# Performance work log

Measured on AMD Instinct MI355X. Metric: run time of the kernel, lower is better.

Reference implementation:

```python
import jax, jax.numpy as jnp
import numpy as np

H = 16   # n_heads == n_I
D = 64   # d_q = d_k = d_v = d_r
DX = H * D
B, S = 4, 2048

def setup_inputs() -> dict:
    key = jax.random.key(0)
    ks = jax.random.split(key, 9)
    sc = 0.02
    return {
        "value": jax.random.normal(ks[0], (B, S, DX), jnp.float32),
        "key":   jax.random.normal(ks[1], (B, S, DX), jnp.float32),
        "query": jax.random.normal(ks[2], (B, S, DX), jnp.float32),
        "Wq_w": jax.random.normal(ks[3], (DX, DX), jnp.float32) * sc,
        "Wq_b": jnp.zeros((DX,), jnp.float32),
        "Wk_w": jax.random.normal(ks[4], (DX, DX), jnp.float32) * sc,
        "Wk_b": jnp.zeros((DX,), jnp.float32),
        "Wv_w": jax.random.normal(ks[5], (DX, DX), jnp.float32) * sc,
        "Wv_b": jnp.zeros((DX,), jnp.float32),
        "Wr_w": jax.random.normal(ks[6], (DX, DX), jnp.float32) * sc,
        "Wr_b": jnp.zeros((DX,), jnp.float32),
        "Wout_w": jax.random.normal(ks[7], (DX, DX), jnp.float32) * sc,
        "Wout_b": jnp.zeros((DX,), jnp.float32),
    }

def _heads(x, b, s):
    # [b, s, H*D] -> [b, H, s, D]
    return x.reshape(b, s, H, D).transpose(0, 2, 1, 3)

def reference(value, key, query, Wq_w, Wq_b, Wk_w, Wk_b, Wv_w, Wv_b,
              Wr_w, Wr_b, Wout_w, Wout_b):
    b, s, _ = query.shape
    # torch nn.Linear: y = x @ W.T + b
    Q = _heads(query @ Wq_w.T + Wq_b, b, s)   # [b,H,s,D]
    K = _heads(key   @ Wk_w.T + Wk_b, b, s)
    V = _heads(value @ Wv_w.T + Wv_b, b, s)
    R = _heads(query @ Wr_w.T + Wr_b, b, s)
    dot_scale = jnp.sqrt(jnp.float32(D))
    scores = jnp.einsum("bhid,bhjd->bhij", Q, K) / dot_scale  # [b,H,s,s]
    attn = jax.nn.softmax(scores, axis=-1)                    # dropout p=0
    out = jnp.einsum("bhij,bhjd->bhid", attn, V)              # [b,H,s,D]
    out = out * R                                             # R-gating
    out = out.transpose(0, 2, 1, 3).reshape(b, s, H * D)
    return out @ Wout_w.T + Wout_b
```

## Files before the change

kernel.cpp:

```cpp
#include <hip/hip_runtime.h>
#include <hip/hip_bf16.h>

typedef __bf16 bf16;
typedef __bf16 bf16x4 __attribute__((ext_vector_type(4)));
typedef __bf16 bf16x8 __attribute__((ext_vector_type(8)));
typedef float  f32x4  __attribute__((ext_vector_type(4)));

#define MFMA_16x16x32(a, b, c) __builtin_amdgcn_mfma_f32_16x16x32_bf16((a), (b), (c), 0, 0, 0)

typedef const void __attribute__((address_space(1))) gvoid;
typedef void __attribute__((address_space(3))) svoid;

__device__ __forceinline__ void async_copy16(const void* gptr, void* ldsptr) {
    __builtin_amdgcn_global_load_lds((gvoid*)gptr, (svoid*)ldsptr, 16, 0, 0);
}

__device__ __forceinline__ int swz8(int row, int quad) {
    return (quad ^ ((row >> 1) & 3)) * 8;
}

__global__ void cvt3_acts(const float* __restrict__ s0, const float* __restrict__ s1,
                          const float* __restrict__ s2,
                          bf16* __restrict__ d0, bf16* __restrict__ d1, bf16* __restrict__ d2)
{
    constexpr int N4SEG = 8192 * 1024 / 4;
    int i = blockIdx.x * blockDim.x + threadIdx.x;
    const int stride = gridDim.x * blockDim.x;
    for (; i < 3 * N4SEG; i += stride) {
        const int seg = i / N4SEG;
        const int j = i - seg * N4SEG;
        const float* s = seg == 0 ? s0 : (seg == 1 ? s1 : s2);
        bf16* d = seg == 0 ? d0 : (seg == 1 ? d1 : d2);
        float4 v = ((const float4*)s)[j];
        bf16x4 o = { (bf16)v.x, (bf16)v.y, (bf16)v.z, (bf16)v.w };
        ((bf16x4*)d)[j] = o;
    }
}

__global__ void cvt5_wts(const float* __restrict__ s0, const float* __restrict__ s1,
                         const float* __restrict__ s2, const float* __restrict__ s3,
                         const float* __restrict__ s4,
                         bf16* __restrict__ d0, bf16* __restrict__ d1, bf16* __restrict__ d2,
                         bf16* __restrict__ d3, bf16* __restrict__ d4)
{
    constexpr int N4SEG = 1024 * 1024 / 4;
    int i = blockIdx.x * blockDim.x + threadIdx.x;
    const int stride = gridDim.x * blockDim.x;
    for (; i < 5 * N4SEG; i += stride) {
        const int seg = i / N4SEG;
        const int j = i - seg * N4SEG;
        const float* s = seg == 0 ? s0 : seg == 1 ? s1 : seg == 2 ? s2 : seg == 3 ? s3 : s4;
        bf16* d = seg == 0 ? d0 : seg == 1 ? d1 : seg == 2 ? d2 : seg == 3 ? d3 : d4;
        float4 v = ((const float4*)s)[j];
        bf16x4 o = { (bf16)v.x, (bf16)v.y, (bf16)v.z, (bf16)v.w };
        ((bf16x4*)d)[j] = o;
    }
}

__global__ void proj_fused(const bf16* __restrict__ xq, const bf16* __restrict__ xk,
                           const bf16* __restrict__ xv, const bf16* __restrict__ wall,
                           const float* __restrict__ ball,
                           bf16* __restrict__ qr, bf16* __restrict__ kws,
                           bf16* __restrict__ vtws)
{
    constexpr int K = 1024, SDIM = 2048;
    __shared__ alignas(16) bf16 As[2][128 * 32];
    __shared__ alignas(16) bf16 Bs[2][128 * 32];

    const int tid  = threadIdx.x;
    const int lane = tid & 63;
    const int wave = tid >> 6;
    const int wm   = wave >> 1;
    const int wn   = wave & 1;
    const int bm   = blockIdx.x * 128;
    const int by   = blockIdx.y;
    const int bn   = by * 128;
    const int l15  = lane & 15;
    const int quad = lane >> 4;

    const bf16* X = (by < 16) ? xq : (by < 24 ? xk : xv);

    const int srow = lane >> 2;
    const int scol = (lane & 3) * 8;

    const bf16* aseg0 = X + (size_t)(bm + wave * 32 + srow) * K + scol;
    const bf16* aseg1 = X + (size_t)(bm + wave * 32 + 16 + srow) * K + scol;
    const bf16* bseg0 = wall + (size_t)(bn + wave * 32 + srow) * K + scol;
    const bf16* bseg1 = wall + (size_t)(bn + wave * 32 + 16 + srow) * K + scol;

    f32x4 acc[4][4] = {};

    async_copy16(aseg0, As[0] + (wave * 2 + 0) * 512);
    async_copy16(aseg1, As[0] + (wave * 2 + 1) * 512);
    async_copy16(bseg0, Bs[0] + (wave * 2 + 0) * 512);
    async_copy16(bseg1, Bs[0] + (wave * 2 + 1) * 512);

    for (int k0 = 0; k0 < K; k0 += 32) {
        const int cur = (k0 >> 5) & 1;
        __syncthreads();
        if (k0 + 32 < K) {
            const int nxt = cur ^ 1;
            async_copy16(aseg0 + k0 + 32, As[nxt] + (wave * 2 + 0) * 512);
            async_copy16(aseg1 + k0 + 32, As[nxt] + (wave * 2 + 1) * 512);
            async_copy16(bseg0 + k0 + 32, Bs[nxt] + (wave * 2 + 0) * 512);
            async_copy16(bseg1 + k0 + 32, Bs[nxt] + (wave * 2 + 1) * 512);
        }

        bf16x8 af[4], bfr[4];
        #pragma unroll
        for (int i = 0; i < 4; ++i)
            af[i] = *(const bf16x8*)(As[cur] + (wm * 64 + i * 16 + l15) * 32 + quad * 8);
        #pragma unroll
        for (int j = 0; j < 4; ++j)
            bfr[j] = *(const bf16x8*)(Bs[cur] + (wn * 64 + j * 16 + l15) * 32 + quad * 8);
        #pragma unroll
        for (int i = 0; i < 4; ++i)
            #pragma unroll
            for (int j = 0; j < 4; ++j)
                acc[i][j] = MFMA_16x16x32(af[i], bfr[j], acc[i][j]);
    }

    #pragma unroll
    for (int i = 0; i < 4; ++i) {
        const int rowg = bm + wm * 64 + i * 16 + quad * 4;
        #pragma unroll
        for (int j = 0; j < 4; ++j) {
            const int colg = bn + wn * 64 + j * 16 + l15;
            const float bv = ball[colg];
            if (by < 16) {
                #pragma unroll
                for (int r = 0; r < 4; ++r)
                    qr[(size_t)(rowg + r) * 2048 + colg] = (bf16)(acc[i][j][r] + bv);
            } else if (by < 24) {
                const int cl = colg - 2048;
                #pragma unroll
                for (int r = 0; r < 4; ++r)
                    kws[(size_t)(rowg + r) * 1024 + cl] = (bf16)(acc[i][j][r] + bv);
            } else {
                const int d = colg - 3072;
                bf16x4 o;
                #pragma unroll
                for (int r = 0; r < 4; ++r) o[r] = (bf16)(acc[i][j][r] + bv);
                *(bf16x4*)(vtws + (size_t)(rowg >> 11) * 1024 * SDIM
                                + (size_t)d * SDIM + (rowg & (SDIM - 1))) = o;
            }
        }
    }
}

__global__ void gemm_out(const bf16* __restrict__ X, const bf16* __restrict__ W,
                         const float* __restrict__ bias, float* __restrict__ Y)
{
    constexpr int K = 1024, N = 1024;
    __shared__ alignas(16) bf16 As[2][128 * 32];
    __shared__ alignas(16) bf16 Bs[2][128 * 32];

    const int tid  = threadIdx.x;
    const int lane = tid & 63;
    const int wave = tid >> 6;
    const int wm   = wave >> 1;
    const int wn   = wave & 1;
    const int bm   = blockIdx.x * 128;
    const int bn   = blockIdx.y * 128;
    const int l15  = lane & 15;
    const int quad = lane >> 4;

    const int srow = lane >> 2;
    const int scol = (lane & 3) * 8;

    const bf16* aseg0 = X + (size_t)(bm + wave * 32 + srow) * K + scol;
    const bf16* aseg1 = X + (size_t)(bm + wave * 32 + 16 + srow) * K + scol;
    const bf16* bseg0 = W + (size_t)(bn + wave * 32 + srow) * K + scol;
    const bf16* bseg1 = W + (size_t)(bn + wave * 32 + 16 + srow) * K + scol;

    f32x4 acc[4][4] = {};

    async_copy16(aseg0, As[0] + (wave * 2 + 0) * 512);
    async_copy16(aseg1, As[0] + (wave * 2 + 1) * 512);
    async_copy16(bseg0, Bs[0] + (wave * 2 + 0) * 512);
    async_copy16(bseg1, Bs[0] + (wave * 2 + 1) * 512);

    for (int k0 = 0; k0 < K; k0 += 32) {
        const int cur = (k0 >> 5) & 1;
        __syncthreads();
        if (k0 + 32 < K) {
            const int nxt = cur ^ 1;
            async_copy16(aseg0 + k0 + 32, As[nxt] + (wave * 2 + 0) * 512);
            async_copy16(aseg1 + k0 + 32, As[nxt] + (wave * 2 + 1) * 512);
            async_copy16(bseg0 + k0 + 32, Bs[nxt] + (wave * 2 + 0) * 512);
            async_copy16(bseg1 + k0 + 32, Bs[nxt] + (wave * 2 + 1) * 512);
        }

        bf16x8 af[4], bfr[4];
        #pragma unroll
        for (int i = 0; i < 4; ++i)
            af[i] = *(const bf16x8*)(As[cur] + (wm * 64 + i * 16 + l15) * 32 + quad * 8);
        #pragma unroll
        for (int j = 0; j < 4; ++j)
            bfr[j] = *(const bf16x8*)(Bs[cur] + (wn * 64 + j * 16 + l15) * 32 + quad * 8);
        #pragma unroll
        for (int i = 0; i < 4; ++i)
            #pragma unroll
            for (int j = 0; j < 4; ++j)
                acc[i][j] = MFMA_16x16x32(af[i], bfr[j], acc[i][j]);
    }

    #pragma unroll
    for (int i = 0; i < 4; ++i) {
        const int rowg = bm + wm * 64 + i * 16 + quad * 4;
        #pragma unroll
        for (int j = 0; j < 4; ++j) {
            const int colg = bn + wn * 64 + j * 16 + l15;
            const float bv = bias[colg];
            #pragma unroll
            for (int r = 0; r < 4; ++r)
                Y[(size_t)(rowg + r) * N + colg] = acc[i][j][r] + bv;
        }
    }
}

__launch_bounds__(256, 4)
__global__ void attn_fused(const bf16* __restrict__ QRp, const bf16* __restrict__ Kp,
                           const bf16* __restrict__ Vtp, bf16* __restrict__ Op)
{
    constexpr int S = 2048, DXc = 1024, QRST = 2048, Dh = 64;
    constexpr int PST = 40;
    constexpr int NT = S / 64;
    __shared__ alignas(16) bf16 Ks[2][2][64 * 32];
    __shared__ alignas(16) bf16 Vt[2][2][64 * 32];
    __shared__ alignas(16) bf16 Pt[4][16 * PST];

    const int tid  = threadIdx.x;
    const int lane = tid & 63;
    const int wave = tid >> 6;
    const int qt = blockIdx.x, h = blockIdx.y, b = blockIdx.z;
    const int l15  = lane & 15;
    const int quad = lane >> 4;

    const size_t qrbase = ((size_t)b * S) * QRST + h * Dh;
    const size_t kbase  = ((size_t)b * S) * DXc + h * Dh;
    const size_t vtbase = ((size_t)(b * 16 + h) * Dh) * S;
    const size_t obase  = ((size_t)b * S) * DXc + h * Dh;

    const int srow = lane >> 2;
    const int scol = ((lane & 3) ^ ((srow >> 1) & 3)) * 8;
    const bf16* kseg = Kp  + kbase  + (size_t)(16 * wave + srow) * DXc + scol;
    const bf16* vseg = Vtp + vtbase + (size_t)(16 * wave + srow) * S   + scol;
    const int soff = wave * 512;

    async_copy16(kseg,      &Ks[0][0][soff]);
    async_copy16(kseg + 32, &Ks[0][1][soff]);
    async_copy16(vseg,      &Vt[0][0][soff]);
    async_copy16(vseg + 32, &Vt[0][1][soff]);

    constexpr float QSCALE = 0.125f * 1.44269504088896340736f;
    bf16x8 qf[2][2];
    #pragma unroll
    for (int mi = 0; mi < 2; ++mi) {
        const int qrow = qt * 128 + wave * 32 + mi * 16 + l15;
        const bf16* qptr = QRp + qrbase + (size_t)qrow * QRST + quad * 8;
        qf[mi][0] = *(const bf16x8*)(qptr);
        qf[mi][1] = *(const bf16x8*)(qptr + 32);
        #pragma unroll
        for (int j = 0; j < 8; ++j) {
            qf[mi][0][j] = (bf16)((float)qf[mi][0][j] * QSCALE);
            qf[mi][1][j] = (bf16)((float)qf[mi][1][j] * QSCALE);
        }
    }

    bf16x8 onef;
    #pragma unroll
    for (int j = 0; j < 8; ++j) onef[j] = (bf16)1.0f;

    f32x4 oacc[2][4] = {};
    f32x4 lsacc[2] = {};

    for (int t = 0; t < NT; ++t) {
        const int cur = t & 1;
        __syncthreads();
        if (t + 1 < NT) {
            const int nxt = cur ^ 1;
            const size_t ko = (size_t)(t + 1) * 64 * DXc;
            const int    vo = (t + 1) * 64;
            async_copy16(kseg + ko,      &Ks[nxt][0][soff]);
            async_copy16(kseg + ko + 32, &Ks[nxt][1][soff]);
            async_copy16(vseg + vo,      &Vt[nxt][0][soff]);
            async_copy16(vseg + vo + 32, &Vt[nxt][1][soff]);
        }

        #pragma unroll
        for (int half = 0; half < 2; ++half) {
            f32x4 st[2][2];
            #pragma unroll
            for (int nbl = 0; nbl < 2; ++nbl) {
                const int nb = half * 2 + nbl;
                bf16x8 kf0 = *(const bf16x8*)(&Ks[cur][0][0] + (nb * 16 + l15) * 32 + swz8(l15, quad));
                bf16x8 kf1 = *(const bf16x8*)(&Ks[cur][1][0] + (nb * 16 + l15) * 32 + swz8(l15, quad));
                #pragma unroll
                for (int mi = 0; mi < 2; ++mi) {
                    f32x4 z = {0.f, 0.f, 0.f, 0.f};
                    z = MFMA_16x16x32(kf1, qf[mi][1], z);
                    st[mi][nbl] = MFMA_16x16x32(kf0, qf[mi][0], z);
                }
            }
            const bf16* vb = &Vt[cur][half][0];
            bf16x8 vtf[4];
            #pragma unroll
            for (int db = 0; db < 4; ++db)
                vtf[db] = *(const bf16x8*)(vb + (db * 16 + l15) * 32 + swz8(l15, quad));
            #pragma unroll
            for (int mi = 0; mi < 2; ++mi) {
                #pragma unroll
                for (int nbl = 0; nbl < 2; ++nbl) {
                    bf16x4 pt;
                    #pragma unroll
                    for (int r = 0; r < 4; ++r)
                        pt[r] = (bf16)__builtin_exp2f(st[mi][nbl][r]);
                    *(bf16x4*)(&Pt[wave][0] + l15 * PST + nbl * 16 + quad * 4) = pt;
                }
                bf16x8 pf = *(const bf16x8*)(&Pt[wave][0] + l15 * PST + quad * 8);
                #pragma unroll
                for (int db = 0; db < 4; ++db)
                    oacc[mi][db] = MFMA_16x16x32(vtf[db], pf, oacc[mi][db]);
                lsacc[mi] = MFMA_16x16x32(onef, pf, lsacc[mi]);
            }
        }
    }

    #pragma unroll
    for (int mi = 0; mi < 2; ++mi) {
        const float inv = 1.0f / lsacc[mi][0];
        const int qrow = qt * 128 + wave * 32 + mi * 16 + l15;
        const bf16* rrow = QRp + qrbase + (size_t)qrow * QRST + 1024;
        bf16* orow = Op + obase + (size_t)qrow * DXc;
        #pragma unroll
        for (int db = 0; db < 4; ++db) {
            bf16x4 rg = *(const bf16x4*)(rrow + db * 16 + quad * 4);
            bf16x4 o;
            #pragma unroll
            for (int r = 0; r < 4; ++r)
                o[r] = (bf16)(oacc[mi][db][r] * inv * (float)rg[r]);
            *(bf16x4*)(orow + db * 16 + quad * 4) = o;
        }
    }
}

extern "C" void kernel_launch(void* const* d_in, const int* in_sizes, int n_in,
                              void* d_out, int out_size, void* d_ws, size_t ws_size,
                              hipStream_t stream)
{
    (void)in_sizes; (void)n_in; (void)out_size; (void)ws_size;
    constexpr int B = 4, S = 2048, DX = 1024, M = B * S;
    constexpr size_t MD = (size_t)M * DX;
    constexpr size_t WD = (size_t)DX * DX;

    const float* value  = (const float*)d_in[0];
    const float* keyi   = (const float*)d_in[1];
    const float* query  = (const float*)d_in[2];
    const float* Wq_w   = (const float*)d_in[3];
    const float* Wq_b   = (const float*)d_in[4];
    const float* Wk_w   = (const float*)d_in[5];
    const float* Wk_b   = (const float*)d_in[6];
    const float* Wv_w   = (const float*)d_in[7];
    const float* Wv_b   = (const float*)d_in[8];
    const float* Wr_w   = (const float*)d_in[9];
    const float* Wr_b   = (const float*)d_in[10];
    const float* Wout_w = (const float*)d_in[11];
    const float* Wout_b = (const float*)d_in[12];

    bf16* p = (bf16*)d_ws;
    bf16* xv   = p;  p += MD;
    bf16* xk   = p;  p += MD;
    bf16* xq   = p;  p += MD;
    bf16* wall = p;  p += 4 * WD;
    bf16* wo   = p;  p += WD;
    bf16* qr   = p;  p += 2 * MD;
    bf16* kws  = p;  p += MD;
    bf16* vtws = p;  p += MD;
    float* ball = (float*)p;
    bf16* ows = xv;

    hipMemcpyAsync(ball,            Wq_b, DX * sizeof(float), hipMemcpyDeviceToDevice, stream);
    hipMemcpyAsync(ball + DX,       Wr_b, DX * sizeof(float), hipMemcpyDeviceToDevice, stream);
    hipMemcpyAsync(ball + 2 * DX,   Wk_b, DX * sizeof(float), hipMemcpyDeviceToDevice, stream);
    hipMemcpyAsync(ball + 3 * DX,   Wv_b, DX * sizeof(float), hipMemcpyDeviceToDevice, stream);

    cvt3_acts<<<dim3(2048), dim3(256), 0, stream>>>(value, keyi, query, xv, xk, xq);
    cvt5_wts <<<dim3(1024), dim3(256), 0, stream>>>(Wq_w, Wr_w, Wk_w, Wv_w, Wout_w,
                                                    wall, wall + WD, wall + 2 * WD,
                                                    wall + 3 * WD, wo);

    proj_fused<<<dim3(M / 128, 32), dim3(256), 0, stream>>>(
        xq, xk, xv, wall, ball, qr, kws, vtws);

    attn_fused<<<dim3(S / 128, 16, B), dim3(256), 0, stream>>>(qr, kws, vtws, ows);

    gemm_out<<<dim3(M / 128, DX / 128), dim3(256), 0, stream>>>(
        ows, wo, Wout_b, (float*)d_out);
}
```

Before: 399.6 us.

## Load V fragments directly from global, batch QK scores and packed bf16 exp

V tiles are no longer staged through LDS via async copies. Each wave now reads its V^T fragments straight from global memory into registers every iteration. All four score blocks are computed before the exponentials, and probabilities are converted with a packed bf16 instruction into a larger per-wave P buffer, so there is no per-half store/reload dependency. Launch bounds are relaxed from 4 to 2 blocks per SM to allow more registers. The costs are more global/L2 traffic for V (each wave loads the full tile redundantly), likely lower occupancy, and global load latency that is not prefetched.

```diff
diff --git a/kernel.cpp b/kernel.cpp
--- a/kernel.cpp
+++ b/kernel.cpp
@@ -17,6 +17,12 @@
 
 __device__ __forceinline__ int swz8(int row, int quad) {
     return (quad ^ ((row >> 1) & 3)) * 8;
+}
+
+__device__ __forceinline__ unsigned cvt_pk_bf16(float a, float b) {
+    unsigned r;
+    asm("v_cvt_pk_bf16_f32 %0, %1, %2" : "=v"(r) : "v"(a), "v"(b));
+    return r;
 }
 
 __global__ void cvt3_acts(const float* __restrict__ s0, const float* __restrict__ s1,
@@ -219,7 +225,7 @@
     }
 }
 
-__launch_bounds__(256, 4)
+__launch_bounds__(256, 2)
 __global__ void attn_fused(const bf16* __restrict__ QRp, const bf16* __restrict__ Kp,
                            const bf16* __restrict__ Vtp, bf16* __restrict__ Op)
 {
@@ -227,8 +233,7 @@
     constexpr int PST = 40;
     constexpr int NT = S / 64;
     __shared__ alignas(16) bf16 Ks[2][2][64 * 32];
-    __shared__ alignas(16) bf16 Vt[2][2][64 * 32];
-    __shared__ alignas(16) bf16 Pt[4][16 * PST];
+    __shared__ alignas(16) bf16 Pt[4][2][2][16 * PST];
 
     const int tid  = threadIdx.x;
     const int lane = tid & 63;
@@ -244,14 +249,13 @@
 
     const int srow = lane >> 2;
     const int scol = ((lane & 3) ^ ((srow >> 1) & 3)) * 8;
-    const bf16* kseg = Kp  + kbase  + (size_t)(16 * wave + srow) * DXc + scol;
-    const bf16* vseg = Vtp + vtbase + (size_t)(16 * wave + srow) * S   + scol;
+    const bf16* kseg = Kp + kbase + (size_t)(16 * wave + srow) * DXc + scol;
     const int soff = wave * 512;
+
+    const bf16* vwp = Vtp + vtbase + (size_t)l15 * S + quad * 8;
 
     async_copy16(kseg,      &Ks[0][0][soff]);
     async_copy16(kseg + 32, &Ks[0][1][soff]);
-    async_copy16(vseg,      &Vt[0][0][soff]);
-    async_copy16(vseg + 32, &Vt[0][1][soff]);
 
     constexpr float QSCALE = 0.125f * 1.44269504088896340736f;
     bf16x8 qf[2][2];
@@ -277,51 +281,59 @@
 
     for (int t = 0; t < NT; ++t) {
         const int cur = t & 1;
+        const int kv0 = t * 64;
         __syncthreads();
         if (t + 1 < NT) {
             const int nxt = cur ^ 1;
             const size_t ko = (size_t)(t + 1) * 64 * DXc;
-            const int    vo = (t + 1) * 64;
             async_copy16(kseg + ko,      &Ks[nxt][0][soff]);
             async_copy16(kseg + ko + 32, &Ks[nxt][1][soff]);
-            async_copy16(vseg + vo,      &Vt[nxt][0][soff]);
-            async_copy16(vseg + vo + 32, &Vt[nxt][1][soff]);
-        }
-
+        }
+
+        bf16x8 vtf[2][4];
+        #pragma unroll
+        for (int half = 0; half < 2; ++half)
+            #pragma unroll
+            for (int db = 0; db < 4; ++db)
+                vtf[half][db] = *(const bf16x8*)(vwp + (size_t)(db * 16) * S
+                                                 + kv0 + half * 32);
+
+        f32x4 st[2][4];
+        #pragma unroll
+        for (int nb = 0; nb < 4; ++nb) {
+            bf16x8 kf0 = *(const bf16x8*)(&Ks[cur][0][0] + (nb * 16 + l15) * 32 + swz8(l15, quad));
+            bf16x8 kf1 = *(const bf16x8*)(&Ks[cur][1][0] + (nb * 16 + l15) * 32 + swz8(l15, quad));
+            #pragma unroll
+            for (int mi = 0; mi < 2; ++mi) {
+                f32x4 z = {0.f, 0.f, 0.f, 0.f};
+                z = MFMA_16x16x32(kf1, qf[mi][1], z);
+                st[mi][nb] = MFMA_16x16x32(kf0, qf[mi][0], z);
+            }
+        }
+        #pragma unroll
+        for (int mi = 0; mi < 2; ++mi) {
+            #pragma unroll
+            for (int nb = 0; nb < 4; ++nb) {
+                const float p0 = __builtin_exp2f(st[mi][nb][0]);
+                const float p1 = __builtin_exp2f(st[mi][nb][1]);
+                const float p2 = __builtin_exp2f(st[mi][nb][2]);
+                const float p3 = __builtin_exp2f(st[mi][nb][3]);
+                uint2 w;
+                w.x = cvt_pk_bf16(p0, p1);
+                w.y = cvt_pk_bf16(p2, p3);
+                *(uint2*)(&Pt[wave][mi][nb >> 1][0] + l15 * PST
+                          + (nb & 1) * 16 + quad * 4) = w;
+            }
+        }
         #pragma unroll
         for (int half = 0; half < 2; ++half) {
-            f32x4 st[2][2];
-            #pragma unroll
-            for (int nbl = 0; nbl < 2; ++nbl) {
-                const int nb = half * 2 + nbl;
-                bf16x8 kf0 = *(const bf16x8*)(&Ks[cur][0][0] + (nb * 16 + l15) * 32 + swz8(l15, quad));
-                bf16x8 kf1 = *(const bf16x8*)(&Ks[cur][1][0] + (nb * 16 + l15) * 32 + swz8(l15, quad));
-                #pragma unroll
-                for (int mi = 0; mi < 2; ++mi) {
-                    f32x4 z = {0.f, 0.f, 0.f, 0.f};
-                    z = MFMA_16x16x32(kf1, qf[mi][1], z);
-                    st[mi][nbl] = MFMA_16x16x32(kf0, qf[mi][0], z);
-                }
-            }
-            const bf16* vb = &Vt[cur][half][0];
-            bf16x8 vtf[4];
-            #pragma unroll
-            for (int db = 0; db < 4; ++db)
-                vtf[db] = *(const bf16x8*)(vb + (db * 16 + l15) * 32 + swz8(l15, quad));
             #pragma unroll
             for (int mi = 0; mi < 2; ++mi) {
-                #pragma unroll
-                for (int nbl = 0; nbl < 2; ++nbl) {
-                    bf16x4 pt;
-                    #pragma unroll
-                    for (int r = 0; r < 4; ++r)
-                        pt[r] = (bf16)__builtin_exp2f(st[mi][nbl][r]);
-                    *(bf16x4*)(&Pt[wave][0] + l15 * PST + nbl * 16 + quad * 4) = pt;
-                }
-                bf16x8 pf = *(const bf16x8*)(&Pt[wave][0] + l15 * PST + quad * 8);
+                bf16x8 pf = *(const bf16x8*)(&Pt[wave][mi][half][0]
+                                             + l15 * PST + quad * 8);
                 #pragma unroll
                 for (int db = 0; db < 4; ++db)
-                    oacc[mi][db] = MFMA_16x16x32(vtf[db], pf, oacc[mi][db]);
+                    oacc[mi][db] = MFMA_16x16x32(vtf[half][db], pf, oacc[mi][db]);
                 lsacc[mi] = MFMA_16x16x32(onef, pf, lsacc[mi]);
             }
         }
```

Result: slower. 480.5 us (+20.2%).
